# Kernel tuning notes

Measured on AMD Instinct MI355X. Metric: run time of the kernel, lower is better.

## Reference

```python
import jax, jax.numpy as jnp
import numpy as np

N_NODES = 50000
N_EDGES = 800000
FEAT = 128
OUT = 128
BATCH = 2


def setup_inputs() -> dict:
    key = jax.random.key(0)
    k_h, k_w1, k_w2, k_a, k_src, k_dst = jax.random.split(key, 6)
    h = jax.random.normal(k_h, (BATCH, N_NODES, FEAT), dtype=jnp.float32)
    # xavier-uniform-ish scale for params
    W1 = jax.random.normal(k_w1, (FEAT, FEAT), dtype=jnp.float32) * (1.414 / np.sqrt(FEAT))
    W2 = jax.random.normal(k_w2, (FEAT, OUT), dtype=jnp.float32) * (1.414 / np.sqrt(FEAT))
    a = jax.random.normal(k_a, (2 * FEAT, 1), dtype=jnp.float32) * 0.05
    src = jax.random.randint(k_src, (N_EDGES,), 0, N_NODES, dtype=jnp.int32)
    dst = jax.random.randint(k_dst, (N_EDGES,), 0, N_NODES, dtype=jnp.int32)
    return {"h": h, "W1": W1, "W2": W2, "a": a, "src": src, "dst": dst}


def reference(h, W1, W2, a, src, dst):
    B, N, F = h.shape
    g = jnp.einsum('bnf,fk->bnk', h, W1)                      # [B,N,F]
    # cat([g_i, g_j]) @ a  ==  g_i @ a[:F] + g_j @ a[F:]
    s_i = g @ a[:F, 0]                                        # [B,N]
    s_j = g @ a[F:, 0]                                        # [B,N]
    e = jax.nn.leaky_relu(s_i[:, src] + s_j[:, dst], 0.2)     # [B,E]
    # segment softmax over edges grouped by src node
    eT = e.T                                                  # [E,B]
    m = jax.ops.segment_max(eT, src, num_segments=N)          # [N,B]
    ex = jnp.exp(eT - m[src])                                 # [E,B]
    denom = jax.ops.segment_sum(ex, src, num_segments=N)      # [N,B]
    alpha = (ex / denom[src]).T                               # [B,E]
    msg = g[:, dst] * alpha[..., None]                        # [B,E,F]
    h_prime = jnp.zeros_like(g).at[:, src].add(msg)           # scatter-add onto src
    return jax.nn.relu(jnp.einsum('bnf,fo->bno', h_prime, W2))
```

## Files before the change

kernel.cpp:

```cpp
#include <hip/hip_runtime.h>
#include <hip/hip_bf16.h>
#include <hip/hip_fp16.h>
#include <cfloat>

#define N_NODES 50000
#define N_EDGES 800000
#define FEAT 128
#define BATCH 2
#define RTOT (BATCH*N_NODES)

typedef __bf16 bf16x8 __attribute__((ext_vector_type(8)));
typedef float  f32x4  __attribute__((ext_vector_type(4)));

__device__ inline unsigned short f2bf(float f){
  unsigned int u = __float_as_uint(f);
  u = (u + 0x7fffu + ((u >> 16) & 1u)) >> 16;
  return (unsigned short)u;
}

__global__ void k_prep(const float* __restrict__ W1, const float* __restrict__ W2,
                       __bf16* __restrict__ W1t, __bf16* __restrict__ W2t,
                       int* __restrict__ cnt){
  int i = blockIdx.x*blockDim.x + threadIdx.x;
  if(i < FEAT*FEAT){
    int k = i >> 7, col = i & 127;
    int sw = (col << 7) + (k ^ ((col & 7) << 3));
    W1t[sw] = (__bf16)W1[i];
    W2t[sw] = (__bf16)W2[i];
  }
  if(i < N_NODES) cnt[i] = 0;
}

__global__ __launch_bounds__(256) void k_gemm1_mfma(const float* __restrict__ h,
        const __bf16* __restrict__ W1t, const float* __restrict__ a,
        __bf16* __restrict__ g, float* __restrict__ s_i, float* __restrict__ s_j,
        const int* __restrict__ src, int* __restrict__ cnt)
{
  __shared__ __bf16 Bs[FEAT*FEAT];
  int t = threadIdx.x, lane = t & 63, wid = t >> 6;
  {
    const float4* srcp = (const float4*)W1t;
    float4* dstp = (float4*)Bs;
    for(int i = t; i < FEAT*FEAT/8; i += 256) dstp[i] = srcp[i];
  }
  __syncthreads();

  int rb = blockIdx.x*64 + wid*16;
  int r  = rb + (lane & 15);
  int kq = (lane >> 4) * 8;

  bf16x8 af[4];
  if(r < RTOT){
    const float* hrow = h + (size_t)r*FEAT + kq;
    #pragma unroll
    for(int ks = 0; ks < 4; ks++){
      float4 p0 = *(const float4*)(hrow + ks*32);
      float4 p1 = *(const float4*)(hrow + ks*32 + 4);
      bf16x8 v;
      v[0]=(__bf16)p0.x; v[1]=(__bf16)p0.y; v[2]=(__bf16)p0.z; v[3]=(__bf16)p0.w;
      v[4]=(__bf16)p1.x; v[5]=(__bf16)p1.y; v[6]=(__bf16)p1.z; v[7]=(__bf16)p1.w;
      af[ks] = v;
    }
  } else {
    #pragma unroll
    for(int ks = 0; ks < 4; ks++){ bf16x8 z = {}; af[ks] = z; }
  }

  f32x4 acc[8] = {};
  #pragma unroll
  for(int cb = 0; cb < 8; cb++){
    int col = cb*16 + (lane & 15);
    int swbase = (col << 7);
    int swx = ((col & 7) << 3);
    #pragma unroll
    for(int ks = 0; ks < 4; ks++){
      int kb = ks*32 + kq;
      bf16x8 bf = *(const bf16x8*)&Bs[swbase + (kb ^ swx)];
      acc[cb] = __builtin_amdgcn_mfma_f32_16x16x32_bf16(af[ks], bf, acc[cb], 0, 0, 0);
    }
  }

  int hgrp = lane >> 4;
  float pi[4] = {0,0,0,0}, pj[4] = {0,0,0,0};
  #pragma unroll
  for(int cb = 0; cb < 8; cb++){
    int col = cb*16 + (lane & 15);
    float al = a[col], ah = a[FEAT + col];
    #pragma unroll
    for(int reg = 0; reg < 4; reg++){
      int row = rb + hgrp*4 + reg;
      float v = acc[cb][reg];
      if(row < RTOT){
        int b = (row >= N_NODES) ? 1 : 0;
        int n = row - b*N_NODES;
        g[(size_t)n*256 + b*128 + col] = (__bf16)v;
      }
      pi[reg] = fmaf(v, al, pi[reg]);
      pj[reg] = fmaf(v, ah, pj[reg]);
    }
  }
  #pragma unroll
  for(int reg = 0; reg < 4; reg++){
    #pragma unroll
    for(int m = 1; m < 16; m <<= 1){
      pi[reg] += __shfl_xor(pi[reg], m, 64);
      pj[reg] += __shfl_xor(pj[reg], m, 64);
    }
  }
  if((lane & 15) == 0){
    #pragma unroll
    for(int reg = 0; reg < 4; reg++){
      int row = rb + hgrp*4 + reg;
      if(row < RTOT){
        int b = (row >= N_NODES) ? 1 : 0;
        int n = row - b*N_NODES;
        s_i[n*2 + b] = pi[reg];
        s_j[n*2 + b] = pj[reg];
      }
    }
  }

  int gs = gridDim.x * 256;
  for(int e = blockIdx.x*256 + t; e < N_EDGES; e += gs)
    atomicAdd(&cnt[src[e]], 1);
}

__global__ __launch_bounds__(1024) void k_scan1(const int* __restrict__ cnt,
                                                int* __restrict__ off, int* __restrict__ bsum){
  __shared__ int s[1024];
  int t = threadIdx.x, idx = blockIdx.x*1024 + t;
  int v = (idx < N_NODES) ? cnt[idx] : 0;
  s[t] = v; __syncthreads();
  for(int st = 1; st < 1024; st <<= 1){
    int u = (t >= st) ? s[t-st] : 0;
    __syncthreads();
    s[t] += u;
    __syncthreads();
  }
  if(idx < N_NODES) off[idx] = s[t] - v;
  if(t == 1023) bsum[blockIdx.x] = s[t];
}
__global__ __launch_bounds__(1024) void k_scan2(int* __restrict__ off,
                                                const int* __restrict__ bsum, int* __restrict__ curs){
  __shared__ int pfx;
  int t = threadIdx.x, idx = blockIdx.x*1024 + t;
  if(t < 64){
    int nb = (N_NODES + 1023)/1024;
    int v0 = (t < nb) ? bsum[t] : 0;
    int v = v0;
    for(int st = 1; st < 64; st <<= 1){
      int u = __shfl_up(v, st, 64);
      if(t >= st) v += u;
    }
    if(t == blockIdx.x) pfx = v - v0;
  }
  __syncthreads();
  if(idx < N_NODES){
    int o = off[idx] + pfx;
    off[idx] = o;
    curs[idx] = o;
  }
}
__global__ void k_fill(const int* __restrict__ src, const int* __restrict__ dst,
                       int* __restrict__ curs, int* __restrict__ dste){
  int e = blockIdx.x*blockDim.x + threadIdx.x;
  if(e < N_EDGES){ int pos = atomicAdd(&curs[src[e]], 1); dste[pos] = dst[e]; }
}

__global__ __launch_bounds__(256) void k_agg(const unsigned int* __restrict__ g,
     const float* __restrict__ s_i, const float* __restrict__ s_j,
     const int* __restrict__ cnt, const int* __restrict__ off,
     const int* __restrict__ dste, unsigned int* __restrict__ hp)
{
  int widb = threadIdx.x>>6, lane = threadIdx.x&63;
  int n = blockIdx.x*4 + widb;
  if(n >= N_NODES) return;
  int deg = cnt[n], o0 = off[n];
  int half = lane >> 5, li = lane & 31;
  float si = s_i[n*2 + half];
  int selp = lane & 32;

  float denom = 0.f;
  float a0=0.f, a1=0.f, a2=0.f, a3=0.f;

  for(int base=0; base<deg; base+=32){
    int i = base + li;
    unsigned int w = 0;
    if(i < deg){
      int d = dste[o0 + i];
      float xx = si + s_j[d*2 + half];
      float x = (xx > 0.f) ? xx : 0.2f*xx;
      float p = __expf(x);
      denom += p;
      w = ((unsigned int)__half_as_ushort(__float2half(p)) << 16) | (unsigned int)d;
    }
    int lim = min(32, deg-base);
    int lim8 = (lim + 7) & ~7;
    for(int j=0; j<lim8; j+=8){
      unsigned int ww[8];
      #pragma unroll
      for(int c=0;c<8;c++) ww[c] = __shfl(w, selp | (j+c), 64);
      uint2 u[8]; float q[8];
      #pragma unroll
      for(int c=0;c<8;c++){
        q[c] = __half2float(__ushort_as_half((unsigned short)(ww[c] >> 16)));
        u[c] = *(const uint2*)(g + (size_t)(ww[c] & 0xffffu)*128 + lane*2);
      }
      #pragma unroll
      for(int c=0;c<8;c++){
        a0 = fmaf(q[c], __uint_as_float(u[c].x << 16),         a0);
        a1 = fmaf(q[c], __uint_as_float(u[c].x & 0xffff0000u), a1);
        a2 = fmaf(q[c], __uint_as_float(u[c].y << 16),         a2);
        a3 = fmaf(q[c], __uint_as_float(u[c].y & 0xffff0000u), a3);
      }
    }
  }
  #pragma unroll
  for(int mm=16; mm; mm>>=1) denom += __shfl_xor(denom, mm, 64);
  float inv = (denom > 0.f) ? 1.0f/denom : 0.f;
  unsigned int w0 = ((unsigned int)f2bf(a1*inv) << 16) | f2bf(a0*inv);
  unsigned int w1 = ((unsigned int)f2bf(a3*inv) << 16) | f2bf(a2*inv);
  uint2 o; o.x = w0; o.y = w1;
  *(uint2*)(hp + (size_t)n*128 + lane*2) = o;
}

__global__ __launch_bounds__(256) void k_gemm2_mfma(const __bf16* __restrict__ hp,
        const __bf16* __restrict__ W2t, float* __restrict__ out)
{
  __shared__ __bf16 Bs[FEAT*FEAT];
  int t = threadIdx.x, lane = t & 63, wid = t >> 6;
  {
    const float4* srcp = (const float4*)W2t;
    float4* dstp = (float4*)Bs;
    for(int i = t; i < FEAT*FEAT/8; i += 256) dstp[i] = srcp[i];
  }
  __syncthreads();

  int rb = blockIdx.x*64 + wid*16;
  int r  = rb + (lane & 15);
  int kq = (lane >> 4) * 8;

  bf16x8 af[4];
  if(r < RTOT){
    const __bf16* hrow = hp + (size_t)r*FEAT + kq;
    #pragma unroll
    for(int ks = 0; ks < 4; ks++) af[ks] = *(const bf16x8*)(hrow + ks*32);
  } else {
    #pragma unroll
    for(int ks = 0; ks < 4; ks++){ bf16x8 z = {}; af[ks] = z; }
  }

  f32x4 acc[8] = {};
  #pragma unroll
  for(int cb = 0; cb < 8; cb++){
    int col = cb*16 + (lane & 15);
    int swbase = (col << 7);
    int swx = ((col & 7) << 3);
    #pragma unroll
    for(int ks = 0; ks < 4; ks++){
      int kb = ks*32 + kq;
      bf16x8 bf = *(const bf16x8*)&Bs[swbase + (kb ^ swx)];
      acc[cb] = __builtin_amdgcn_mfma_f32_16x16x32_bf16(af[ks], bf, acc[cb], 0, 0, 0);
    }
  }

  int hgrp = lane >> 4;
  #pragma unroll
  for(int cb = 0; cb < 8; cb++){
    int col = cb*16 + (lane & 15);
    #pragma unroll
    for(int reg = 0; reg < 4; reg++){
      int ri = rb + hgrp*4 + reg;
      if(ri < RTOT){
        int orow = (ri & 1)*N_NODES + (ri >> 1);
        out[(size_t)orow*FEAT + col] = fmaxf(acc[cb][reg], 0.f);
      }
    }
  }
}

extern "C" void kernel_launch(void* const* d_in, const int* in_sizes, int n_in,
                              void* d_out, int out_size, void* d_ws, size_t ws_size,
                              hipStream_t stream) {
  const float* h  = (const float*)d_in[0];
  const float* W1 = (const float*)d_in[1];
  const float* W2 = (const float*)d_in[2];
  const float* a  = (const float*)d_in[3];
  const int* src  = (const int*)d_in[4];
  const int* dst  = (const int*)d_in[5];
  float* out = (float*)d_out;

  char* w = (char*)d_ws;
  __bf16* g   = (__bf16*)w;                          w += (size_t)RTOT*FEAT*2;
  __bf16* hp  = (__bf16*)w;                          w += (size_t)RTOT*FEAT*2;
  float* s_i  = (float*)w;                           w += (size_t)RTOT*4;
  float* s_j  = (float*)w;                           w += (size_t)RTOT*4;
  __bf16* W1t = (__bf16*)w;                          w += FEAT*FEAT*2;
  __bf16* W2t = (__bf16*)w;                          w += FEAT*FEAT*2;
  int* cnt  = (int*)w;                               w += N_NODES*4;
  int* off  = (int*)w;                               w += N_NODES*4;
  int* curs = (int*)w;                               w += N_NODES*4;
  int* dste = (int*)w;                               w += N_EDGES*4;
  int* bsum = (int*)w;

  k_prep<<<(N_NODES+255)/256,256,0,stream>>>(W1,W2,W1t,W2t,cnt);

  int gemm_grid = (RTOT + 63)/64;
  k_gemm1_mfma<<<gemm_grid,256,0,stream>>>(h,W1t,a,g,s_i,s_j,src,cnt);

  int nb = (N_NODES+1023)/1024;
  k_scan1<<<nb,1024,0,stream>>>(cnt,off,bsum);
  k_scan2<<<nb,1024,0,stream>>>(off,bsum,curs);
  k_fill<<<(N_EDGES+255)/256,256,0,stream>>>(src,dst,curs,dste);

  k_agg<<<(N_NODES+3)/4,256,0,stream>>>((const unsigned int*)g,s_i,s_j,cnt,off,dste,(unsigned int*)hp);

  k_gemm2_mfma<<<gemm_grid,256,0,stream>>>(hp,W2t,out);
}
```

Measured before the change: 181.7 us.

## Fuse edge aggregation with second GEMM via shared-memory h' tile

Merges the aggregation kernel and the W2 GEMM into one kernel. Each 512-thread block aggregates 8 nodes (16 batch rows) into a swizzled LDS tile, then each wave computes one 16-column MFMA slice against W2 held in LDS. This drops the global round trip of the bf16 h' buffer and one launch. In exchange every block reloads the 32KB W2 into LDS, uses more shared memory per block, and the GEMM stage waits behind the slowest node's aggregation.

New measurement: 166.4 us. 1.09x faster.

```diff
diff --git a/kernel.cpp b/kernel.cpp
--- a/kernel.cpp
+++ b/kernel.cpp
@@ -167,14 +167,22 @@
   if(e < N_EDGES){ int pos = atomicAdd(&curs[src[e]], 1); dste[pos] = dst[e]; }
 }
 
-__global__ __launch_bounds__(256) void k_agg(const unsigned int* __restrict__ g,
+__global__ __launch_bounds__(512) void k_agg2(const unsigned int* __restrict__ g,
      const float* __restrict__ s_i, const float* __restrict__ s_j,
      const int* __restrict__ cnt, const int* __restrict__ off,
-     const int* __restrict__ dste, unsigned int* __restrict__ hp)
+     const int* __restrict__ dste, const __bf16* __restrict__ W2t,
+     float* __restrict__ out)
 {
-  int widb = threadIdx.x>>6, lane = threadIdx.x&63;
-  int n = blockIdx.x*4 + widb;
-  if(n >= N_NODES) return;
+  __shared__ __bf16 Bs[FEAT*FEAT];
+  __shared__ __bf16 hpT[16*FEAT];
+  int t = threadIdx.x, lane = t & 63, w = t >> 6;
+  {
+    const float4* srcp = (const float4*)W2t;
+    float4* dstp = (float4*)Bs;
+    for(int i = t; i < FEAT*FEAT/8; i += 512) dstp[i] = srcp[i];
+  }
+
+  int n = blockIdx.x*8 + w;
   int deg = cnt[n], o0 = off[n];
   int half = lane >> 5, li = lane & 31;
   float si = s_i[n*2 + half];
@@ -185,21 +193,21 @@
 
   for(int base=0; base<deg; base+=32){
     int i = base + li;
-    unsigned int w = 0;
+    unsigned int wv = 0;
     if(i < deg){
       int d = dste[o0 + i];
       float xx = si + s_j[d*2 + half];
       float x = (xx > 0.f) ? xx : 0.2f*xx;
       float p = __expf(x);
       denom += p;
-      w = ((unsigned int)__half_as_ushort(__float2half(p)) << 16) | (unsigned int)d;
+      wv = ((unsigned int)__half_as_ushort(__float2half(p)) << 16) | (unsigned int)d;
     }
     int lim = min(32, deg-base);
     int lim8 = (lim + 7) & ~7;
     for(int j=0; j<lim8; j+=8){
       unsigned int ww[8];
       #pragma unroll
-      for(int c=0;c<8;c++) ww[c] = __shfl(w, selp | (j+c), 64);
+      for(int c=0;c<8;c++) ww[c] = __shfl(wv, selp | (j+c), 64);
       uint2 u[8]; float q[8];
       #pragma unroll
       for(int c=0;c<8;c++){
@@ -218,64 +226,45 @@
   #pragma unroll
   for(int mm=16; mm; mm>>=1) denom += __shfl_xor(denom, mm, 64);
   float inv = (denom > 0.f) ? 1.0f/denom : 0.f;
-  unsigned int w0 = ((unsigned int)f2bf(a1*inv) << 16) | f2bf(a0*inv);
-  unsigned int w1 = ((unsigned int)f2bf(a3*inv) << 16) | f2bf(a2*inv);
-  uint2 o; o.x = w0; o.y = w1;
-  *(uint2*)(hp + (size_t)n*128 + lane*2) = o;
-}
-
-__global__ __launch_bounds__(256) void k_gemm2_mfma(const __bf16* __restrict__ hp,
-        const __bf16* __restrict__ W2t, float* __restrict__ out)
-{
-  __shared__ __bf16 Bs[FEAT*FEAT];
-  int t = threadIdx.x, lane = t & 63, wid = t >> 6;
+
   {
-    const float4* srcp = (const float4*)W2t;
-    float4* dstp = (float4*)Bs;
-    for(int i = t; i < FEAT*FEAT/8; i += 256) dstp[i] = srcp[i];
+    int ri = w*2 + half;
+    int gidx = li >> 1;
+    int gsw = gidx ^ (ri & 7);
+    int coff = gsw*8 + (li & 1)*4;
+    unsigned int w0 = ((unsigned int)f2bf(a1*inv) << 16) | f2bf(a0*inv);
+    unsigned int w1 = ((unsigned int)f2bf(a3*inv) << 16) | f2bf(a2*inv);
+    uint2 o; o.x = w0; o.y = w1;
+    *(uint2*)&hpT[ri*FEAT + coff] = o;
   }
   __syncthreads();
 
-  int rb = blockIdx.x*64 + wid*16;
-  int r  = rb + (lane & 15);
-  int kq = (lane >> 4) * 8;
-
+  int r  = lane & 15;
+  int kq16 = lane >> 4;
   bf16x8 af[4];
-  if(r < RTOT){
-    const __bf16* hrow = hp + (size_t)r*FEAT + kq;
-    #pragma unroll
-    for(int ks = 0; ks < 4; ks++) af[ks] = *(const bf16x8*)(hrow + ks*32);
-  } else {
-    #pragma unroll
-    for(int ks = 0; ks < 4; ks++){ bf16x8 z = {}; af[ks] = z; }
-  }
-
-  f32x4 acc[8] = {};
-  #pragma unroll
-  for(int cb = 0; cb < 8; cb++){
-    int col = cb*16 + (lane & 15);
-    int swbase = (col << 7);
-    int swx = ((col & 7) << 3);
-    #pragma unroll
-    for(int ks = 0; ks < 4; ks++){
-      int kb = ks*32 + kq;
-      bf16x8 bf = *(const bf16x8*)&Bs[swbase + (kb ^ swx)];
-      acc[cb] = __builtin_amdgcn_mfma_f32_16x16x32_bf16(af[ks], bf, acc[cb], 0, 0, 0);
-    }
-  }
-
+  #pragma unroll
+  for(int ks = 0; ks < 4; ks++){
+    int gr = ks*4 + kq16;
+    int gsw2 = gr ^ (r & 7);
+    af[ks] = *(const bf16x8*)&hpT[r*FEAT + gsw2*8];
+  }
+  f32x4 acc = {};
+  int col = w*16 + (lane & 15);
+  int swbase = (col << 7);
+  int swx = ((col & 7) << 3);
+  #pragma unroll
+  for(int ks = 0; ks < 4; ks++){
+    int kb = ks*32 + kq16*8;
+    bf16x8 bf = *(const bf16x8*)&Bs[swbase + (kb ^ swx)];
+    acc = __builtin_amdgcn_mfma_f32_16x16x32_bf16(af[ks], bf, acc, 0, 0, 0);
+  }
   int hgrp = lane >> 4;
   #pragma unroll
-  for(int cb = 0; cb < 8; cb++){
-    int col = cb*16 + (lane & 15);
-    #pragma unroll
-    for(int reg = 0; reg < 4; reg++){
-      int ri = rb + hgrp*4 + reg;
-      if(ri < RTOT){
-        int orow = (ri & 1)*N_NODES + (ri >> 1);
-        out[(size_t)orow*FEAT + col] = fmaxf(acc[cb][reg], 0.f);
-      }
-    }
+  for(int reg = 0; reg < 4; reg++){
+    int rri = hgrp*4 + reg;
+    int node = blockIdx.x*8 + (rri >> 1);
+    int b = rri & 1;
+    out[(size_t)(b*N_NODES + node)*FEAT + col] = fmaxf(acc[reg], 0.f);
   }
 }
 
@@ -292,7 +281,6 @@
 
   char* w = (char*)d_ws;
   __bf16* g   = (__bf16*)w;                          w += (size_t)RTOT*FEAT*2;
-  __bf16* hp  = (__bf16*)w;                          w += (size_t)RTOT*FEAT*2;
   float* s_i  = (float*)w;                           w += (size_t)RTOT*4;
   float* s_j  = (float*)w;                           w += (size_t)RTOT*4;
   __bf16* W1t = (__bf16*)w;                          w += FEAT*FEAT*2;
@@ -313,7 +301,5 @@
   k_scan2<<<nb,1024,0,stream>>>(off,bsum,curs);
   k_fill<<<(N_EDGES+255)/256,256,0,stream>>>(src,dst,curs,dste);
 
-  k_agg<<<(N_NODES+3)/4,256,0,stream>>>((const unsigned int*)g,s_i,s_j,cnt,off,dste,(unsigned int*)hp);
-
-  k_gemm2_mfma<<<gemm_grid,256,0,stream>>>(hp,W2t,out);
-}
+  k_agg2<<<N_NODES/8,512,0,stream>>>((const unsigned int*)g,s_i,s_j,cnt,off,dste,W2t,out);
+}
```
